# Optimization experiments

Measured on AMD Instinct MI355X. Metric: run time of the kernel, lower is better.

The kernel has to match this reference:

```python
import jax, jax.numpy as jnp
import numpy as np

BS, C, H, W = 2, 128, 80, 160
P, G = 9, 8
GC = C // G
EPS = 1e-5


def _layernorm_c(x, g, b):
    # x: (bs, C, H, W); LayerNorm over channel dim (to_3d dim=2 -> norm over c)
    m = jnp.mean(x, axis=1, keepdims=True)
    v = jnp.mean((x - m) ** 2, axis=1, keepdims=True)
    return (x - m) / jnp.sqrt(v + EPS) * g[None, :, None, None] + b[None, :, None, None]


def _conv1x1(x, w, b):
    return jnp.einsum('bchw,oc->bohw', x, w) + b[None, :, None, None]


def _bilinear_sample(feat, pts):
    # feat (bs,C,H,W); pts (bs,N,2) normalized [0,1]; zero padding outside (DAF convention)
    bs, c, h, w = feat.shape
    x = pts[..., 0] * w - 0.5
    y = pts[..., 1] * h - 0.5
    x0 = jnp.floor(x)
    y0 = jnp.floor(y)
    dx = x - x0
    dy = y - y0
    x0i = x0.astype(jnp.int32)
    y0i = y0.astype(jnp.int32)

    def corner(xi, yi, wgt):
        valid = (xi >= 0) & (xi < w) & (yi >= 0) & (yi < h)
        xc = jnp.clip(xi, 0, w - 1)
        yc = jnp.clip(yi, 0, h - 1)
        g = jax.vmap(lambda f, yy, xx: f[:, yy, xx].T)(feat, yc, xc)  # (bs,N,C)
        return g * (wgt * valid)[..., None]

    return (corner(x0i, y0i, (1 - dx) * (1 - dy))
            + corner(x0i + 1, y0i, dx * (1 - dy))
            + corner(x0i, y0i + 1, (1 - dx) * dy)
            + corner(x0i + 1, y0i + 1, dx * dy))


def _branch(match_flat, anchor, feat_value, wmap, kp_w, kp_b):
    bs = feat_value.shape[0]
    hw = H * W
    # Sparse1DKeyPointsGenerator: learned 1D offsets along the disparity (x) direction
    off = match_flat @ kp_w.T + kp_b  # (bs, HW, P)
    anc = anchor.reshape(bs, hw, P, 2)
    kp = jnp.stack([anc[..., 0] + off, anc[..., 1]], axis=-1)  # (bs,HW,P,2)
    # group-softmax attention weights over num_pts
    wts = wmap.transpose(0, 2, 3, 1).reshape(bs, hw, P, G)  # channel c = p*G + g
    wts = jax.nn.softmax(wts, axis=2)
    # deformable aggregation: bilinear gather at key points + group-weighted sum over pts
    sampled = _bilinear_sample(feat_value, kp.reshape(bs, hw * P, 2))
    sampled = sampled.reshape(bs, hw, P, G, GC)
    out = jnp.einsum('bnpgc,bnpg->bngc', sampled, wts).reshape(bs, hw, C)
    out = out.reshape(bs, H, W, C).transpose(0, 3, 1, 2)
    return out, kp


def _forward(mask, match, context, geometric, context_anchor_points, geometric_anchor_points,
             ln_g, ln_b, lnc_g, lnc_b, lng_g, lng_b,
             wc_w, wc_b, wg_w, wg_b, vc_w, vc_b, vg_w, vg_b,
             out_w, out_b, kpc_w, kpc_b, kpg_w, kpg_b):
    bs = match.shape[0]
    hw = H * W
    match_n = _layernorm_c(match, ln_g, ln_b)
    context_n = _layernorm_c(context, lnc_g, lnc_b)
    geometric_n = _layernorm_c(geometric, lng_g, lng_b)
    ctx_val = _conv1x1(context_n, vc_w, vc_b)
    geo_val = _conv1x1(geometric_n, vg_w, vg_b)
    match_flat = match_n.reshape(bs, C, hw).transpose(0, 2, 1)  # (bs,HW,C)
    wc = _conv1x1(match_n, wc_w, wc_b)  # (bs,G*P,H,W)
    wg = _conv1x1(match_n, wg_w, wg_b)
    ctx_out, ctx_kp = _branch(match_flat, context_anchor_points, ctx_val, wc, kpc_w, kpc_b)
    geo_out, geo_kp = _branch(match_flat, geometric_anchor_points, geo_val, wg, kpg_w, kpg_b)
    out = jnp.concatenate([ctx_out * mask, geo_out], axis=1)
    out = _conv1x1(out, out_w, out_b)  # proj_drop is identity (p=0)
    return out, ctx_kp.reshape(bs, H, W, P, 2), geo_kp.reshape(bs, H, W, P, 2)


def setup_inputs() -> dict:
    key = jax.random.key(0)
    ks = jax.random.split(key, 20)

    def wn(k, shape):
        return jax.random.normal(k, shape, jnp.float32) * 0.02

    return {
        'mask': jax.random.uniform(ks[0], (BS, 1, H, W), jnp.float32),
        'match': jax.random.normal(ks[1], (BS, C, H, W), jnp.float32),
        'context': jax.random.normal(ks[2], (BS, C, H, W), jnp.float32),
        'geometric': jax.random.normal(ks[3], (BS, C, H, W), jnp.float32),
        'context_anchor_points': jax.random.uniform(ks[4], (BS, H, W, P, 2), jnp.float32),
        'geometric_anchor_points': jax.random.uniform(ks[5], (BS, H, W, P, 2), jnp.float32),
        'ln_g': jnp.ones((C,), jnp.float32), 'ln_b': jnp.zeros((C,), jnp.float32),
        'lnc_g': jnp.ones((C,), jnp.float32), 'lnc_b': jnp.zeros((C,), jnp.float32),
        'lng_g': jnp.ones((C,), jnp.float32), 'lng_b': jnp.zeros((C,), jnp.float32),
        'wc_w': wn(ks[6], (G * P, C)), 'wc_b': jnp.zeros((G * P,), jnp.float32),
        'wg_w': wn(ks[7], (G * P, C)), 'wg_b': jnp.zeros((G * P,), jnp.float32),
        'vc_w': wn(ks[8], (C, C)), 'vc_b': jnp.zeros((C,), jnp.float32),
        'vg_w': wn(ks[9], (C, C)), 'vg_b': jnp.zeros((C,), jnp.float32),
        'out_w': wn(ks[10], (C, 2 * C)), 'out_b': jnp.zeros((C,), jnp.float32),
        'kpc_w': wn(ks[11], (P, C)), 'kpc_b': jnp.zeros((P,), jnp.float32),
        'kpg_w': wn(ks[12], (P, C)), 'kpg_b': jnp.zeros((P,), jnp.float32),
    }


def reference(mask, match, context, geometric, context_anchor_points, geometric_anchor_points,
              ln_g, ln_b, lnc_g, lnc_b, lng_g, lng_b,
              wc_w, wc_b, wg_w, wg_b, vc_w, vc_b, vg_w, vg_b,
              out_w, out_b, kpc_w, kpc_b, kpg_w, kpg_b):
    return _forward(mask, match, context, geometric, context_anchor_points, geometric_anchor_points,
                    ln_g, ln_b, lnc_g, lnc_b, lng_g, lng_b,
                    wc_w, wc_b, wg_w, wg_b, vc_w, vc_b, vg_w, vg_b,
                    out_w, out_b, kpc_w, kpc_b, kpg_w, kpg_b)
```

## Files before the change

### kernel.cpp

```cpp
#include <hip/hip_runtime.h>
#include <hip/hip_bf16.h>

typedef __hip_bfloat16 bf16;
typedef __bf16 b16x8 __attribute__((ext_vector_type(8)));
typedef float f32x4 __attribute__((ext_vector_type(4)));
typedef float f32x2 __attribute__((ext_vector_type(2)));

#define HWs   12800
#define NPIX  25600
#define IMG_H 80
#define IMG_W 160

#define OFF_VCB  0
#define OFF_VGB  16384
#define OFF_MATB 32768
#define OFF_OUTB 53504
#define NW_BF16  86272

static __device__ inline unsigned char enc_fp8(float v)
{
    return (unsigned char)(__builtin_amdgcn_cvt_pk_fp8_f32(v, v, 0, false) & 0xFF);
}

__global__ __launch_bounds__(256) void k_prep(
    const float* __restrict__ vc_w, const float* __restrict__ vg_w,
    const float* __restrict__ wc_w, const float* __restrict__ wg_w,
    const float* __restrict__ kpc_w, const float* __restrict__ kpg_w,
    const float* __restrict__ out_w,
    const float* __restrict__ wc_b, const float* __restrict__ wg_b,
    const float* __restrict__ kpc_b, const float* __restrict__ kpg_b,
    bf16* __restrict__ wbuf, float* __restrict__ bias176)
{
    int i = blockIdx.x * 256 + threadIdx.x;
    if (i < 16384) {
        wbuf[i] = __float2bfloat16(vc_w[i]);
    } else if (i < 32768) {
        wbuf[i] = __float2bfloat16(vg_w[i - 16384]);
    } else if (i < 53504) {
        int j = i - 32768; int row = j >> 7; int c = j & 127;
        float v;
        if (row < 72)       v = wc_w[row * 128 + c];
        else if (row < 144) v = wg_w[(row - 72) * 128 + c];
        else if (row < 153) v = kpc_w[(row - 144) * 128 + c];
        else                v = kpg_w[(row - 153) * 128 + c];
        wbuf[i] = __float2bfloat16(v);
    } else if (i < NW_BF16) {
        wbuf[i] = __float2bfloat16(out_w[i - 53504]);
    } else if (i < NW_BF16 + 176) {
        int j = i - NW_BF16;
        float v = 0.f;
        if (j < 72)       v = wc_b[j];
        else if (j < 144) v = wg_b[j - 72];
        else if (j < 153) v = kpc_b[j - 144];
        else if (j < 162) v = kpg_b[j - 153];
        bias176[j] = v;
    }
}

__global__ __launch_bounds__(256) void k_stage1(
    const float* __restrict__ match, const float* __restrict__ context, const float* __restrict__ geometric,
    const float* __restrict__ ln_g, const float* __restrict__ ln_b,
    const float* __restrict__ lnc_g, const float* __restrict__ lnc_b,
    const float* __restrict__ lng_g, const float* __restrict__ lng_b,
    const float* __restrict__ vc_b, const float* __restrict__ vg_b,
    const bf16* __restrict__ wbuf, const float* __restrict__ bias176,
    const float* __restrict__ anc_c, const float* __restrict__ anc_g,
    unsigned char* __restrict__ ctx8, unsigned char* __restrict__ geo8,
    bf16* __restrict__ wts_g, float* __restrict__ coords_g,
    float* __restrict__ kp_out)
{
    __shared__ __align__(16) bf16 tile_s[32 * 136];
    __shared__ bf16 logit_s[32 * 144];
    __shared__ float offs_s[32 * 18];
    __shared__ float red1[8][32];
    __shared__ float red2[8][32];

    int bx = blockIdx.x;
    int seg = bx / 800;
    int tile = bx - seg * 800;
    int t = threadIdx.x;
    int pixbase = tile * 32;

    const float* X  = (seg == 0) ? context : (seg == 1) ? geometric : match;
    const float* gg = (seg == 0) ? lnc_g   : (seg == 1) ? lng_g     : ln_g;
    const float* bb = (seg == 0) ? lnc_b   : (seg == 1) ? lng_b     : ln_b;

    int p = t & 31;
    int cq = t >> 5;
    int b = pixbase >= HWs;
    int hw0 = pixbase - b * HWs;
    const float* base = X + ((size_t)b * 128) * HWs + hw0 + p;
    float xv[16];
#pragma unroll
    for (int j = 0; j < 16; j++) xv[j] = base[(size_t)(cq * 16 + j) * HWs];

    int wv = t >> 6;
    int lane = t & 63;
    int s = wv >> 1;
    int h = wv & 1;
    int lrow = lane & 15;
    int lq = lane >> 4;
    const bf16* Wb = (seg == 0) ? wbuf + OFF_VCB
                   : (seg == 1) ? wbuf + OFF_VGB
                                : wbuf + OFF_MATB;
    b16x8 wf[4][4];
    float bpre[4];
#pragma unroll
    for (int i = 0; i < 4; i++) {
        int o = (h + 2 * i) * 16 + lrow;
        const bf16* wr = Wb + (size_t)o * 128;
#pragma unroll
        for (int kk = 0; kk < 4; kk++)
            wf[i][kk] = *(const b16x8*)(wr + (kk * 4 + lq) * 8);
        bpre[i] = (seg == 0) ? vc_b[o] : (seg == 1) ? vg_b[o] : bias176[o];
    }

    {
        float s1 = 0.f, s2 = 0.f;
#pragma unroll
        for (int j = 0; j < 16; j++) { s1 += xv[j]; s2 += xv[j] * xv[j]; }
        red1[cq][p] = s1; red2[cq][p] = s2;
        __syncthreads();
        float S1 = 0.f, S2 = 0.f;
#pragma unroll
        for (int q = 0; q < 8; q++) { S1 += red1[q][p]; S2 += red2[q][p]; }
        float mean = S1 * (1.f / 128.f);
        float var  = fmaxf(S2 * (1.f / 128.f) - mean * mean, 0.f);
        float rstd = rsqrtf(var + 1e-5f);
#pragma unroll
        for (int j = 0; j < 16; j++) {
            int c = cq * 16 + j;
            float y = (xv[j] - mean) * rstd * gg[c] + bb[c];
            tile_s[p * 136 + c] = __float2bfloat16(y);
        }
        __syncthreads();
    }

    const b16x8* arow = (const b16x8*)(tile_s + (s * 16 + lrow) * 136);
    b16x8 af[4];
#pragma unroll
    for (int kk = 0; kk < 4; kk++) af[kk] = arow[kk * 4 + lq];

    if (seg < 2) {
        unsigned char* val = (seg == 0) ? ctx8 : geo8;
#pragma unroll
        for (int i = 0; i < 4; i++) {
            int o = (h + 2 * i) * 16 + lrow;
            f32x4 acc = {0.f, 0.f, 0.f, 0.f};
#pragma unroll
            for (int kk = 0; kk < 4; kk++)
                acc = __builtin_amdgcn_mfma_f32_16x16x32_bf16(af[kk], wf[i][kk], acc, 0, 0, 0);
#pragma unroll
            for (int r = 0; r < 4; r++) {
                int pix = pixbase + s * 16 + lq * 4 + r;
                val[(size_t)pix * 128 + o] = enc_fp8(acc[r] + bpre[i]);
            }
        }
        return;
    }

#pragma unroll
    for (int i = 0; i < 4; i++) {
        int o = (h + 2 * i) * 16 + lrow;
        f32x4 acc = {0.f, 0.f, 0.f, 0.f};
#pragma unroll
        for (int kk = 0; kk < 4; kk++)
            acc = __builtin_amdgcn_mfma_f32_16x16x32_bf16(af[kk], wf[i][kk], acc, 0, 0, 0);
#pragma unroll
        for (int r = 0; r < 4; r++) {
            int row = s * 16 + lq * 4 + r;
            logit_s[row * 144 + o] = __float2bfloat16(acc[r] + bpre[i]);
        }
    }
    for (int ot = h + 8; ot < 11; ot += 2) {
        int o = ot * 16 + lrow;
        const bf16* wr = Wb + (size_t)o * 128;
        f32x4 acc = {0.f, 0.f, 0.f, 0.f};
#pragma unroll
        for (int kk = 0; kk < 4; kk++)
            acc = __builtin_amdgcn_mfma_f32_16x16x32_bf16(af[kk], *(const b16x8*)(wr + (kk * 4 + lq) * 8), acc, 0, 0, 0);
        float bias = bias176[o];
#pragma unroll
        for (int r = 0; r < 4; r++) {
            int row = s * 16 + lq * 4 + r;
            float v = acc[r] + bias;
            if (o < 144)       logit_s[row * 144 + o] = __float2bfloat16(v);
            else if (o < 162)  offs_s[row * 18 + (o - 144)] = v;
        }
    }
    __syncthreads();

#pragma unroll
    for (int i = 0; i < 2; i++) {
        int task = t + 256 * i;
        int lp = task >> 4;
        int sub = task & 15;
        int br = sub >> 3;
        int g = sub & 7;
        const bf16* basel = logit_s + lp * 144 + br * 72 + g;
        float v[9];
        float m = -1e30f;
#pragma unroll
        for (int pp = 0; pp < 9; pp++) { v[pp] = __bfloat162float(basel[pp * 8]); m = fmaxf(m, v[pp]); }
        float ssum = 0.f;
#pragma unroll
        for (int pp = 0; pp < 9; pp++) { v[pp] = __expf(v[pp] - m); ssum += v[pp]; }
        float inv = 1.f / ssum;
        int pix = pixbase + lp;
        bf16* wbp = wts_g + ((size_t)pix * 2 + br) * 72 + g * 9;
#pragma unroll
        for (int pp = 0; pp < 9; pp++) wbp[pp] = __float2bfloat16(v[pp] * inv);
    }

    for (int i = 0; i < 3; i++) {
        int task = t + 256 * i;
        if (task < 576) {
            int lp = task / 18;
            int sub = task - lp * 18;
            int br = sub / 9;
            int pp = sub - br * 9;
            int pix = pixbase + lp;
            float off = offs_s[lp * 18 + br * 9 + pp];
            const float* anc = br ? anc_g : anc_c;
            float ax = anc[(size_t)pix * 18 + pp * 2];
            float ay = anc[(size_t)pix * 18 + pp * 2 + 1];
            float kx = ax + off;
            float* kpo = kp_out + (size_t)br * (NPIX * 18) + (size_t)pix * 18 + pp * 2;
            kpo[0] = kx;
            kpo[1] = ay;
            float* cbp = coords_g + ((size_t)pix * 2 + br) * 18 + pp * 2;
            cbp[0] = kx * 160.f - 0.5f;
            cbp[1] = ay * 80.f - 0.5f;
        }
    }
}

__global__ __launch_bounds__(256) void k_agg(
    const unsigned char* __restrict__ ctx8, const unsigned char* __restrict__ geo8,
    const bf16* __restrict__ wts_g, const float* __restrict__ coords_g,
    const float* __restrict__ mask,
    bf16* __restrict__ aggf)
{
    int t = threadIdx.x;
    int wv = t >> 6;
    int lane = t & 63;
    int q = lane >> 4;
    int sub = lane & 15;
    int c0 = sub * 8;
    int g = sub >> 1;

    int bx = blockIdx.x;
    int xcd = bx & 7;
    int br = xcd >> 2;
    int grp = (bx >> 3) * 4 + (xcd & 3);
    int pix = grp * 16 + wv * 4 + q;
    int tk = pix * 2 + br;
    int b = pix >= HWs;
    int rowbase = b * HWs;

    const unsigned char* val = br ? geo8 : ctx8;
    const float* cb = coords_g + (size_t)tk * 18;
    const bf16* wb = wts_g + (size_t)tk * 72 + g * 9;

    float wtv[9];
#pragma unroll
    for (int pp = 0; pp < 9; pp++) wtv[pp] = __bfloat162float(wb[pp]);

    f32x2 acc2[4] = {{0.f, 0.f}, {0.f, 0.f}, {0.f, 0.f}, {0.f, 0.f}};
    for (int pp = 0; pp < 9; pp++) {
        float px = cb[pp * 2];
        float py = cb[pp * 2 + 1];
        float fx = floorf(px), fy = floorf(py);
        float dx = px - fx, dy = py - fy;
        int x0 = (int)fx, y0 = (int)fy;
        float wt = wtv[pp];
#pragma unroll
        for (int c4 = 0; c4 < 4; c4++) {
            int xi = x0 + (c4 & 1);
            int yi = y0 + (c4 >> 1);
            bool ok = (xi >= 0) & (xi < IMG_W) & (yi >= 0) & (yi < IMG_H);
            int xc = min(max(xi, 0), IMG_W - 1);
            int yc = min(max(yi, 0), IMG_H - 1);
            float wx = (c4 & 1) ? dx : 1.f - dx;
            float wy = (c4 >> 1) ? dy : 1.f - dy;
            float wgt = ok ? wx * wy * wt : 0.f;
            f32x2 w2 = {wgt, wgt};
            uint2 u = *(const uint2*)(val + (size_t)(rowbase + yc * IMG_W + xc) * 128 + c0);
            acc2[0] += w2 * __builtin_amdgcn_cvt_pk_f32_fp8(u.x, false);
            acc2[1] += w2 * __builtin_amdgcn_cvt_pk_f32_fp8(u.x, true);
            acc2[2] += w2 * __builtin_amdgcn_cvt_pk_f32_fp8(u.y, false);
            acc2[3] += w2 * __builtin_amdgcn_cvt_pk_f32_fp8(u.y, true);
        }
    }
    float mv = (br == 0) ? mask[pix] : 1.f;
    b16x8 pk;
#pragma unroll
    for (int j = 0; j < 8; j++) pk[j] = (__bf16)(acc2[j >> 1][j & 1] * mv);
    *(b16x8*)(aggf + (size_t)pix * 256 + br * 128 + c0) = pk;
}

__global__ __launch_bounds__(256) void k_out(
    const bf16* __restrict__ aggf,
    const bf16* __restrict__ outb, const float* __restrict__ out_b,
    float* __restrict__ out)
{
    __shared__ float ot_s[128 * 33];
    int t = threadIdx.x;
    int pixbase = blockIdx.x * 32;
    int wv = t >> 6;
    int lane = t & 63;
    int s = wv >> 1;
    int h = wv & 1;
    int lrow = lane & 15;
    int lq = lane >> 4;
    const b16x8* arow = (const b16x8*)(aggf + (size_t)(pixbase + s * 16 + lrow) * 256);
    b16x8 af[8];
#pragma unroll
    for (int kk = 0; kk < 8; kk++) af[kk] = arow[kk * 4 + lq];
    int b = pixbase >= HWs;
#pragma unroll
    for (int i = 0; i < 4; i++) {
        int o = (h + 2 * i) * 16 + lrow;
        const bf16* wrow = outb + (size_t)o * 256;
        f32x4 acc = {0.f, 0.f, 0.f, 0.f};
#pragma unroll
        for (int kk = 0; kk < 8; kk++)
            acc = __builtin_amdgcn_mfma_f32_16x16x32_bf16(af[kk], *(const b16x8*)(wrow + (kk * 4 + lq) * 8), acc, 0, 0, 0);
        float bias = out_b[o];
#pragma unroll
        for (int r = 0; r < 4; r++)
            ot_s[o * 33 + (s * 16 + lq * 4 + r)] = acc[r] + bias;
    }
    __syncthreads();

    int row = t >> 1;
    int ch0 = (t & 1) * 16;
    int hwb = pixbase - b * HWs;
    float* orow = out + (size_t)b * (128 * HWs) + (size_t)row * HWs + hwb + ch0;
    const float* srow = ot_s + row * 33 + ch0;
#pragma unroll
    for (int j = 0; j < 4; j++) {
        float4 v = {srow[4 * j], srow[4 * j + 1], srow[4 * j + 2], srow[4 * j + 3]};
        *(float4*)(orow + 4 * j) = v;
    }
}

extern "C" void kernel_launch(void* const* d_in, const int* in_sizes, int n_in,
                              void* d_out, int out_size, void* d_ws, size_t ws_size,
                              hipStream_t stream)
{
    const float* mask      = (const float*)d_in[0];
    const float* match     = (const float*)d_in[1];
    const float* context   = (const float*)d_in[2];
    const float* geometric = (const float*)d_in[3];
    const float* anc_c     = (const float*)d_in[4];
    const float* anc_g     = (const float*)d_in[5];
    const float* ln_g  = (const float*)d_in[6];
    const float* ln_b  = (const float*)d_in[7];
    const float* lnc_g = (const float*)d_in[8];
    const float* lnc_b = (const float*)d_in[9];
    const float* lng_g = (const float*)d_in[10];
    const float* lng_b = (const float*)d_in[11];
    const float* wc_w  = (const float*)d_in[12];
    const float* wc_b  = (const float*)d_in[13];
    const float* wg_w  = (const float*)d_in[14];
    const float* wg_b  = (const float*)d_in[15];
    const float* vc_w  = (const float*)d_in[16];
    const float* vc_b  = (const float*)d_in[17];
    const float* vg_w  = (const float*)d_in[18];
    const float* vg_b  = (const float*)d_in[19];
    const float* out_w = (const float*)d_in[20];
    const float* out_b = (const float*)d_in[21];
    const float* kpc_w = (const float*)d_in[22];
    const float* kpc_b = (const float*)d_in[23];
    const float* kpg_w = (const float*)d_in[24];
    const float* kpg_b = (const float*)d_in[25];

    char* w = (char*)d_ws;
    unsigned char* ctx8 = (unsigned char*)(w);
    unsigned char* geo8 = (unsigned char*)(w + 3276800);
    bf16*  wts_g    = (bf16*)(w + 6553600);
    float* coords_g = (float*)(w + 13926400);
    bf16*  aggf     = (bf16*)(w + 17612800);
    bf16*  wbuf     = (bf16*)(w + 30720000);
    float* bias176  = (float*)(w + 30892544);

    float* outp = (float*)d_out;
    float* kp_out = outp + (size_t)2 * 128 * HWs;

    k_prep<<<(NW_BF16 + 176 + 255) / 256, 256, 0, stream>>>(
        vc_w, vg_w, wc_w, wg_w, kpc_w, kpg_w, out_w,
        wc_b, wg_b, kpc_b, kpg_b, wbuf, bias176);
    k_stage1<<<2400, 256, 0, stream>>>(match, context, geometric,
                                       ln_g, ln_b, lnc_g, lnc_b, lng_g, lng_b,
                                       vc_b, vg_b, wbuf, bias176,
                                       anc_c, anc_g,
                                       ctx8, geo8, wts_g, coords_g, kp_out);
    k_agg<<<3200, 256, 0, stream>>>(ctx8, geo8, wts_g, coords_g, mask, aggf);
    k_out<<<800, 256, 0, stream>>>(aggf, wbuf + OFF_OUTB, out_b, outp);
}
```

Measured before the change: 205.7 us.

## Make stage1 wave-independent: per-wave 16-pixel tiles with shuffle-based layernorm

Restructures k_stage1 so each wavefront owns 16 pixels and computes all output channels itself. The LayerNorm reduction moves from shared memory to cross-lane shuffles, and the per-wave shared-memory slices remove every __syncthreads. Weights are now streamed from global memory per output tile instead of being preloaded into registers, which adds repeated weight loads per wave. The grid is halved to 1200 blocks of 64 pixels each, and the normalized tile is written to shared memory with vectorized stores.

New measurement: 207.9 us. Within noise of the previous version (+1.1%).

```diff
diff --git a/kernel.cpp b/kernel.cpp
--- a/kernel.cpp
+++ b/kernel.cpp
@@ -57,6 +57,7 @@
     }
 }
 
+#define WPITCH 5760
 __global__ __launch_bounds__(256) void k_stage1(
     const float* __restrict__ match, const float* __restrict__ context, const float* __restrict__ geometric,
     const float* __restrict__ ln_g, const float* __restrict__ ln_b,
@@ -69,110 +70,88 @@
     bf16* __restrict__ wts_g, float* __restrict__ coords_g,
     float* __restrict__ kp_out)
 {
-    __shared__ __align__(16) bf16 tile_s[32 * 136];
-    __shared__ bf16 logit_s[32 * 144];
-    __shared__ float offs_s[32 * 18];
-    __shared__ float red1[8][32];
-    __shared__ float red2[8][32];
+    __shared__ __align__(16) char sm[4 * WPITCH];
 
     int bx = blockIdx.x;
-    int seg = bx / 800;
-    int tile = bx - seg * 800;
+    int seg = bx / 400;
+    int tile = bx - seg * 400;
     int t = threadIdx.x;
-    int pixbase = tile * 32;
+    int wv = t >> 6;
+    int lane = t & 63;
+    int pixbase = tile * 64 + wv * 16;
 
     const float* X  = (seg == 0) ? context : (seg == 1) ? geometric : match;
     const float* gg = (seg == 0) ? lnc_g   : (seg == 1) ? lng_g     : ln_g;
     const float* bb = (seg == 0) ? lnc_b   : (seg == 1) ? lng_b     : ln_b;
 
-    int p = t & 31;
-    int cq = t >> 5;
+    int p = lane & 15;
+    int cq = lane >> 4;
     int b = pixbase >= HWs;
     int hw0 = pixbase - b * HWs;
-    const float* base = X + ((size_t)b * 128) * HWs + hw0 + p;
-    float xv[16];
-#pragma unroll
-    for (int j = 0; j < 16; j++) xv[j] = base[(size_t)(cq * 16 + j) * HWs];
-
-    int wv = t >> 6;
-    int lane = t & 63;
-    int s = wv >> 1;
-    int h = wv & 1;
+    const float* base = X + ((size_t)b * 128 + cq * 32) * HWs + hw0 + p;
+    float xv[32];
+#pragma unroll
+    for (int j = 0; j < 32; j++) xv[j] = base[(size_t)j * HWs];
+
+    float s1 = 0.f, s2 = 0.f;
+#pragma unroll
+    for (int j = 0; j < 32; j++) { s1 += xv[j]; s2 += xv[j] * xv[j]; }
+    s1 += __shfl_xor(s1, 16); s2 += __shfl_xor(s2, 16);
+    s1 += __shfl_xor(s1, 32); s2 += __shfl_xor(s2, 32);
+    float mean = s1 * (1.f / 128.f);
+    float var  = fmaxf(s2 * (1.f / 128.f) - mean * mean, 0.f);
+    float rstd = rsqrtf(var + 1e-5f);
+
+    bf16* tile_s = (bf16*)(sm + wv * WPITCH);
+    {
+        b16x8 w0, w1, w2, w3;
+#pragma unroll
+        for (int j = 0; j < 8; j++) {
+            int c = cq * 32;
+            w0[j] = (__bf16)((xv[j]      - mean) * rstd * gg[c + j]      + bb[c + j]);
+            w1[j] = (__bf16)((xv[j + 8]  - mean) * rstd * gg[c + j + 8]  + bb[c + j + 8]);
+            w2[j] = (__bf16)((xv[j + 16] - mean) * rstd * gg[c + j + 16] + bb[c + j + 16]);
+            w3[j] = (__bf16)((xv[j + 24] - mean) * rstd * gg[c + j + 24] + bb[c + j + 24]);
+        }
+        b16x8* dst = (b16x8*)(tile_s + p * 136 + cq * 32);
+        dst[0] = w0; dst[1] = w1; dst[2] = w2; dst[3] = w3;
+    }
+
     int lrow = lane & 15;
     int lq = lane >> 4;
+    const b16x8* arow = (const b16x8*)(tile_s + lrow * 136);
+    b16x8 af[4];
+#pragma unroll
+    for (int kk = 0; kk < 4; kk++) af[kk] = arow[kk * 4 + lq];
+
     const bf16* Wb = (seg == 0) ? wbuf + OFF_VCB
                    : (seg == 1) ? wbuf + OFF_VGB
                                 : wbuf + OFF_MATB;
-    b16x8 wf[4][4];
-    float bpre[4];
-#pragma unroll
-    for (int i = 0; i < 4; i++) {
-        int o = (h + 2 * i) * 16 + lrow;
-        const bf16* wr = Wb + (size_t)o * 128;
-#pragma unroll
-        for (int kk = 0; kk < 4; kk++)
-            wf[i][kk] = *(const b16x8*)(wr + (kk * 4 + lq) * 8);
-        bpre[i] = (seg == 0) ? vc_b[o] : (seg == 1) ? vg_b[o] : bias176[o];
-    }
-
-    {
-        float s1 = 0.f, s2 = 0.f;
-#pragma unroll
-        for (int j = 0; j < 16; j++) { s1 += xv[j]; s2 += xv[j] * xv[j]; }
-        red1[cq][p] = s1; red2[cq][p] = s2;
-        __syncthreads();
-        float S1 = 0.f, S2 = 0.f;
-#pragma unroll
-        for (int q = 0; q < 8; q++) { S1 += red1[q][p]; S2 += red2[q][p]; }
-        float mean = S1 * (1.f / 128.f);
-        float var  = fmaxf(S2 * (1.f / 128.f) - mean * mean, 0.f);
-        float rstd = rsqrtf(var + 1e-5f);
-#pragma unroll
-        for (int j = 0; j < 16; j++) {
-            int c = cq * 16 + j;
-            float y = (xv[j] - mean) * rstd * gg[c] + bb[c];
-            tile_s[p * 136 + c] = __float2bfloat16(y);
-        }
-        __syncthreads();
-    }
-
-    const b16x8* arow = (const b16x8*)(tile_s + (s * 16 + lrow) * 136);
-    b16x8 af[4];
-#pragma unroll
-    for (int kk = 0; kk < 4; kk++) af[kk] = arow[kk * 4 + lq];
 
     if (seg < 2) {
+        const float* Bv = (seg == 0) ? vc_b : vg_b;
         unsigned char* val = (seg == 0) ? ctx8 : geo8;
 #pragma unroll
-        for (int i = 0; i < 4; i++) {
-            int o = (h + 2 * i) * 16 + lrow;
+        for (int ot = 0; ot < 8; ot++) {
+            int o = ot * 16 + lrow;
+            const bf16* wr = Wb + (size_t)o * 128;
             f32x4 acc = {0.f, 0.f, 0.f, 0.f};
 #pragma unroll
             for (int kk = 0; kk < 4; kk++)
-                acc = __builtin_amdgcn_mfma_f32_16x16x32_bf16(af[kk], wf[i][kk], acc, 0, 0, 0);
+                acc = __builtin_amdgcn_mfma_f32_16x16x32_bf16(af[kk], *(const b16x8*)(wr + (kk * 4 + lq) * 8), acc, 0, 0, 0);
+            float bias = Bv[o];
 #pragma unroll
             for (int r = 0; r < 4; r++) {
-                int pix = pixbase + s * 16 + lq * 4 + r;
-                val[(size_t)pix * 128 + o] = enc_fp8(acc[r] + bpre[i]);
+                int pix = pixbase + lq * 4 + r;
+                val[(size_t)pix * 128 + o] = enc_fp8(acc[r] + bias);
             }
         }
         return;
     }
 
-#pragma unroll
-    for (int i = 0; i < 4; i++) {
-        int o = (h + 2 * i) * 16 + lrow;
-        f32x4 acc = {0.f, 0.f, 0.f, 0.f};
-#pragma unroll
-        for (int kk = 0; kk < 4; kk++)
-            acc = __builtin_amdgcn_mfma_f32_16x16x32_bf16(af[kk], wf[i][kk], acc, 0, 0, 0);
-#pragma unroll
-        for (int r = 0; r < 4; r++) {
-            int row = s * 16 + lq * 4 + r;
-            logit_s[row * 144 + o] = __float2bfloat16(acc[r] + bpre[i]);
-        }
-    }
-    for (int ot = h + 8; ot < 11; ot += 2) {
+    bf16* logit_s = (bf16*)(sm + wv * WPITCH);
+    float* offs_s = (float*)(sm + wv * WPITCH + 4608);
+    for (int ot = 0; ot < 11; ot++) {
         int o = ot * 16 + lrow;
         const bf16* wr = Wb + (size_t)o * 128;
         f32x4 acc = {0.f, 0.f, 0.f, 0.f};
@@ -182,17 +161,16 @@
         float bias = bias176[o];
 #pragma unroll
         for (int r = 0; r < 4; r++) {
-            int row = s * 16 + lq * 4 + r;
+            int row = lq * 4 + r;
             float v = acc[r] + bias;
             if (o < 144)       logit_s[row * 144 + o] = __float2bfloat16(v);
             else if (o < 162)  offs_s[row * 18 + (o - 144)] = v;
         }
     }
-    __syncthreads();
-
-#pragma unroll
-    for (int i = 0; i < 2; i++) {
-        int task = t + 256 * i;
+
+#pragma unroll
+    for (int i = 0; i < 4; i++) {
+        int task = lane + 64 * i;
         int lp = task >> 4;
         int sub = task & 15;
         int br = sub >> 3;
@@ -212,9 +190,9 @@
         for (int pp = 0; pp < 9; pp++) wbp[pp] = __float2bfloat16(v[pp] * inv);
     }
 
-    for (int i = 0; i < 3; i++) {
-        int task = t + 256 * i;
-        if (task < 576) {
+    for (int i = 0; i < 5; i++) {
+        int task = lane + 64 * i;
+        if (task < 288) {
             int lp = task / 18;
             int sub = task - lp * 18;
             int br = sub / 9;
@@ -391,7 +369,7 @@
     k_prep<<<(NW_BF16 + 176 + 255) / 256, 256, 0, stream>>>(
         vc_w, vg_w, wc_w, wg_w, kpc_w, kpg_w, out_w,
         wc_b, wg_b, kpc_b, kpg_b, wbuf, bias176);
-    k_stage1<<<2400, 256, 0, stream>>>(match, context, geometric,
+    k_stage1<<<1200, 256, 0, stream>>>(match, context, geometric,
                                        ln_g, ln_b, lnc_g, lnc_b, lng_g, lng_b,
                                        vc_b, vg_b, wbuf, bias176,
                                        anc_c, anc_g,
```
